# Kernel optimization log

Measured on AMD Instinct MI355X. Metric: run time of the kernel, lower is better.

## Reference

```python
import jax, jax.numpy as jnp
import numpy as np

B, C, N, H = 2, 512, 2048, 8
DK = C // H  # 64


def entmax15(z):
    """Exact 1.5-entmax over last axis (Peters & Martins 2019, sort-based)."""
    z = z / 2.0
    z = z - jnp.max(z, axis=-1, keepdims=True)
    zs = -jnp.sort(-z, axis=-1)  # descending sort
    n = zs.shape[-1]
    rho = jnp.arange(1, n + 1, dtype=z.dtype)
    mean = jnp.cumsum(zs, axis=-1) / rho
    mean_sq = jnp.cumsum(zs * zs, axis=-1) / rho
    ss = rho * (mean_sq - mean * mean)
    delta = (1.0 - ss) / rho
    tau = mean - jnp.sqrt(jnp.clip(delta, 1e-12))
    support = jnp.sum((tau <= zs).astype(jnp.int32), axis=-1)
    tau_star = jnp.take_along_axis(tau, (support - 1)[..., None], axis=-1)
    return jnp.square(jnp.clip(z - tau_star, 0.0))


def layernorm(x, a, b, eps=1e-6):
    # matches the custom LayerNorm: unbiased std (torch default), eps added to std
    mean = jnp.mean(x, axis=-1, keepdims=True)
    std = jnp.sqrt(jnp.var(x, axis=-1, ddof=1, keepdims=True))
    return a * (x - mean) / (std + eps) + b


def setup_inputs() -> dict:
    key = jax.random.key(0)
    ks = jax.random.split(key, 7)
    s = 1.0 / np.sqrt(C)  # torch Linear init range
    u = lambda k, shp: jax.random.uniform(k, shp, jnp.float32, -s, s)
    return {
        "x": jax.random.normal(ks[0], (B, C, N), jnp.float32),
        "Wq": u(ks[1], (C, C)), "bq": u(ks[2], (C,)),
        "Wk": u(ks[3], (C, C)), "bk": u(ks[4], (C,)),
        "Wv": u(ks[5], (C, C)), "bv": u(ks[6], (C,)),
        "a2": jnp.ones((C,), jnp.float32),
        "b2": jnp.ones((C,), jnp.float32),
    }


def reference(x, Wq, bq, Wk, bk, Wv, bv, a2, b2):
    xt = jnp.transpose(x, (0, 2, 1))  # (B, N, C)
    x_res = xt

    def heads(W, bias):
        y = xt @ W.T + bias  # torch Linear: x @ W.T + b
        return jnp.transpose(y.reshape(B, N, H, DK), (0, 2, 1, 3))  # (B,H,N,DK)

    q, k, v = heads(Wq, bq), heads(Wk, bk), heads(Wv, bv)
    energy = jnp.einsum("bhqd,bhkd->bhqk", q, k) / np.sqrt(DK)
    p = entmax15(energy)  # sparse attention weights
    o = jnp.einsum("bhqk,bhkd->bhqd", p, v)
    o = jnp.transpose(o, (0, 2, 1, 3)).reshape(B, N, C)
    # dropouts are identity in eval mode
    return x_res + layernorm(o, a2, b2)
```

## Files before the change

### kernel.cpp

```cpp
#include <hip/hip_runtime.h>

typedef _Float16 f16;
typedef _Float16 f16x2 __attribute__((ext_vector_type(2)));
typedef _Float16 f16x4 __attribute__((ext_vector_type(4)));
typedef _Float16 f16x8 __attribute__((ext_vector_type(8)));
typedef float    f32x4 __attribute__((ext_vector_type(4)));

#define B_  2
#define C_  512
#define N_  2048
#define H_  8
#define DK_ 64
#define BH_ 16
#define NIT 8

static __device__ __forceinline__ f16x2 cvt_pk(float a, float b) {
  return __builtin_bit_cast(f16x2, __builtin_amdgcn_cvt_pkrtz(a, b));
}

#if defined(__has_builtin)
#if __has_builtin(__builtin_amdgcn_fdot2)
#define FDOT2(a,b,c) __builtin_amdgcn_fdot2((a),(b),(c),false)
#endif
#endif
#ifndef FDOT2
static __device__ __forceinline__ float FDOT2(f16x2 a, f16x2 b, float c) {
  return c + (float)a[0]*(float)b[0] + (float)a[1]*(float)b[1];
}
#endif

#define MFMA16(a,b,acc) __builtin_amdgcn_mfma_f32_16x16x32_f16((a),(b),(acc),0,0,0)

__global__ __launch_bounds__(256) void prep_x(const float* __restrict__ x,
                                              f16* __restrict__ xT)
{
  const int nt = blockIdx.x, mt = blockIdx.y, b = blockIdx.z;
  const int n0 = nt * 64, m0 = mt * 64;
  __shared__ float tile[64][65];
  const int t = threadIdx.x;
  {
    const int ml = t >> 2, nc = (t & 3) * 16;
    const float* src = x + ((size_t)(b * C_ + m0 + ml)) * N_ + n0 + nc;
    *(float4*)&tile[ml][nc]      = *(const float4*)(src);
    *(float4*)&tile[ml][nc + 4]  = *(const float4*)(src + 4);
    *(float4*)&tile[ml][nc + 8]  = *(const float4*)(src + 8);
    *(float4*)&tile[ml][nc + 12] = *(const float4*)(src + 12);
  }
  __syncthreads();
  {
    const int nl = t >> 2, mc = (t & 3) * 16;
    f16x8 o0, o1;
    #pragma unroll
    for (int i = 0; i < 8; ++i) {
      o0[i] = (f16)tile[mc + i][nl];
      o1[i] = (f16)tile[mc + 8 + i][nl];
    }
    f16* dst = xT + ((size_t)(b * N_ + n0 + nl)) * C_ + m0 + mc;
    *(f16x8*)(dst)     = o0;
    *(f16x8*)(dst + 8) = o1;
  }
}

__global__ __launch_bounds__(256) void qkv_lds(
    const f16* __restrict__ xT,
    const float* __restrict__ Wq, const float* __restrict__ Wk,
    const float* __restrict__ Wv,
    const float* __restrict__ bq, const float* __restrict__ bk,
    const float* __restrict__ bv,
    f16* __restrict__ q16, f16* __restrict__ k16, f16* __restrict__ vT16)
{
  const int nt = blockIdx.x, ctb = blockIdx.y, z = blockIdx.z;
  const int b = z / 3, mat = z % 3;
  const float* W    = (mat == 0) ? Wq : (mat == 1) ? Wk : Wv;
  const float* bias = (mat == 0) ? bq : (mat == 1) ? bk : bv;
  const int n0 = nt * 128, c0 = ctb * 64;

  __shared__ f16 As[128 * 64];
  __shared__ f16 Bs[64 * 64];

  const int t = threadIdx.x, w = t >> 6, lane = t & 63;
  const int c = lane & 15, g = lane >> 4;

  const int rB0 = t >> 3, dS = t & 7;
  const int rB1 = rB0 + 32;
  const f16* aSrc[4];
  #pragma unroll
  for (int u = 0; u < 4; ++u) {
    const int r = rB0 + 32 * u;
    aSrc[u] = xT + (size_t)(b * N_ + n0 + r) * C_ + 8 * (dS ^ (r & 7));
  }
  const float* wSrc0 = W + (size_t)(c0 + rB0) * C_ + 8 * (dS ^ (rB0 & 7));
  const float* wSrc1 = W + (size_t)(c0 + rB1) * C_ + 8 * (dS ^ (rB1 & 7));

  f32x4 acc[2][4] = {};
  #pragma unroll 1
  for (int k0 = 0; k0 < C_; k0 += 64) {
    #pragma unroll
    for (int u = 0; u < 4; ++u)
      *(f16x8*)&As[(rB0 + 32 * u) * 64 + 8 * dS] = *(const f16x8*)(aSrc[u] + k0);
    {
      float4 u0 = *(const float4*)(wSrc0 + k0);
      float4 u1 = *(const float4*)(wSrc0 + k0 + 4);
      union { f16x8 v8; f16x2 v2[4]; } u;
      u.v2[0] = cvt_pk(u0.x, u0.y); u.v2[1] = cvt_pk(u0.z, u0.w);
      u.v2[2] = cvt_pk(u1.x, u1.y); u.v2[3] = cvt_pk(u1.z, u1.w);
      *(f16x8*)&Bs[rB0 * 64 + 8 * dS] = u.v8;
    }
    {
      float4 u0 = *(const float4*)(wSrc1 + k0);
      float4 u1 = *(const float4*)(wSrc1 + k0 + 4);
      union { f16x8 v8; f16x2 v2[4]; } u;
      u.v2[0] = cvt_pk(u0.x, u0.y); u.v2[1] = cvt_pk(u0.z, u0.w);
      u.v2[2] = cvt_pk(u1.x, u1.y); u.v2[3] = cvt_pk(u1.z, u1.w);
      *(f16x8*)&Bs[rB1 * 64 + 8 * dS] = u.v8;
    }
    __syncthreads();
    const int ar0 = 32 * w + c, ar1 = ar0 + 16;
    f16x8 a00 = *(const f16x8*)&As[ar0 * 64 + 8 * (g ^ (ar0 & 7))];
    f16x8 a01 = *(const f16x8*)&As[ar0 * 64 + 8 * ((4 + g) ^ (ar0 & 7))];
    f16x8 a10 = *(const f16x8*)&As[ar1 * 64 + 8 * (g ^ (ar1 & 7))];
    f16x8 a11 = *(const f16x8*)&As[ar1 * 64 + 8 * ((4 + g) ^ (ar1 & 7))];
    #pragma unroll
    for (int ct = 0; ct < 4; ++ct) {
      const int br = ct * 16 + c;
      f16x8 b0 = *(const f16x8*)&Bs[br * 64 + 8 * (g ^ (br & 7))];
      f16x8 b1 = *(const f16x8*)&Bs[br * 64 + 8 * ((4 + g) ^ (br & 7))];
      acc[0][ct] = MFMA16(a00, b0, acc[0][ct]);
      acc[0][ct] = MFMA16(a01, b1, acc[0][ct]);
      acc[1][ct] = MFMA16(a10, b0, acc[1][ct]);
      acc[1][ct] = MFMA16(a11, b1, acc[1][ct]);
    }
    __syncthreads();
  }

  #pragma unroll
  for (int rf = 0; rf < 2; ++rf) {
    const int nOut = n0 + 32 * w + 16 * rf + 4 * g;
    #pragma unroll
    for (int ct = 0; ct < 4; ++ct) {
      const int ccol = c0 + ct * 16 + c;
      const float bb = bias[ccol];
      if (mat == 2) {
        const int base = n0 + 32 * w;
        f16* vrow = vT16 + ((size_t)(b * C_ + ccol)) * N_ + base + 8 * g + rf;
        #pragma unroll
        for (int e = 0; e < 4; ++e)
          vrow[2 * e] = (f16)(acc[rf][ct][e] + bb);
      } else {
        const int h = ccol >> 6, d = ccol & 63;
        f16* out = (mat == 0) ? q16 : k16;
        const float sc = (mat == 0) ? 0.0625f : 1.0f;
        #pragma unroll
        for (int e = 0; e < 4; ++e)
          out[((size_t)((b * H_ + h) * N_ + nOut + e)) * DK_ + d] =
              (f16)((acc[rf][ct][e] + bb) * sc);
      }
    }
  }
}

__global__ __launch_bounds__(256, 4) void attn(
    const f16* __restrict__ q16, const f16* __restrict__ k16,
    const f16* __restrict__ vT16, float* __restrict__ o)
{
  const int bh = blockIdx.y;
  const int n0 = blockIdx.x * 16;
  const int t = threadIdx.x;
  const int w = t >> 6, lane = t & 63;
  const int c = lane & 15, g = lane >> 4;

  __shared__ f16 p_lds[16 * 520];
  __shared__ float red[2][4][16][2];

  const f16* Q  = q16  + (size_t)bh * N_ * DK_;
  const f16* K  = k16  + (size_t)bh * N_ * DK_;
  const f16* VT = vT16 + (size_t)bh * DK_ * N_;

  f16x8 qa0 = *(const f16x8*)(Q + (size_t)(n0 + c) * DK_ + 8 * g);
  f16x8 qa1 = *(const f16x8*)(Q + (size_t)(n0 + c) * DK_ + 32 + 8 * g);

  const int jbase = w * 512;

  f16x2 z2[64];
  #pragma unroll
  for (int tt = 0; tt < 16; ++tt) {
    const f16* kp0 = K + (size_t)(jbase + 32 * tt + c) * DK_ + 8 * g;
    f16x8 kb00 = *(const f16x8*)(kp0);
    f16x8 kb01 = *(const f16x8*)(kp0 + 32);
    f16x8 kb10 = *(const f16x8*)(kp0 + 16 * DK_);
    f16x8 kb11 = *(const f16x8*)(kp0 + 16 * DK_ + 32);
    f32x4 a0 = {}, a1 = {};
    a0 = MFMA16(qa0, kb00, a0);
    a0 = MFMA16(qa1, kb01, a0);
    a1 = MFMA16(qa0, kb10, a1);
    a1 = MFMA16(qa1, kb11, a1);
    #pragma unroll
    for (int e = 0; e < 4; ++e)
      z2[tt * 4 + e] = cvt_pk(a0[e], a1[e]);
  }

  f16x2 m2[4];
  #pragma unroll
  for (int e = 0; e < 4; ++e) m2[e] = z2[e];
  #pragma unroll
  for (int tt = 1; tt < 16; ++tt)
    #pragma unroll
    for (int e = 0; e < 4; ++e)
      m2[e] = __builtin_elementwise_max(m2[e], z2[tt * 4 + e]);
  float m[4];
  #pragma unroll
  for (int e = 0; e < 4; ++e) m[e] = fmaxf((float)m2[e][0], (float)m2[e][1]);
  #pragma unroll
  for (int dm = 1; dm <= 8; dm <<= 1)
    #pragma unroll
    for (int e = 0; e < 4; ++e) m[e] = fmaxf(m[e], __shfl_xor(m[e], dm, 64));
  if (c == 0) {
    #pragma unroll
    for (int e = 0; e < 4; ++e) red[0][w][4 * g + e][0] = m[e];
  }
  __syncthreads();
  #pragma unroll
  for (int e = 0; e < 4; ++e) {
    const int r = 4 * g + e;
    m[e] = fmaxf(fmaxf(red[0][0][r][0], red[0][1][r][0]),
                 fmaxf(red[0][2][r][0], red[0][3][r][0]));
  }

  float tau[4];
  #pragma unroll
  for (int e = 0; e < 4; ++e) tau[e] = m[e] - 1.f;

  const f16x2 one2  = {(_Float16)1.f, (_Float16)1.f};
  const f16x2 zero2 = {(_Float16)0.f, (_Float16)0.f};

  #pragma unroll 1
  for (int it = 0; it < NIT; ++it) {
    const int pb = (it + 1) & 1;
    f16x2 tau2[4];
    #pragma unroll
    for (int e = 0; e < 4; ++e)
      tau2[e] = cvt_pk(tau[e], tau[e]);
    float S1[4] = {0.f, 0.f, 0.f, 0.f}, S2[4] = {0.f, 0.f, 0.f, 0.f};
    #pragma unroll
    for (int tt = 0; tt < 16; ++tt)
      #pragma unroll
      for (int e = 0; e < 4; ++e) {
        f16x2 d2 = z2[tt * 4 + e] - tau2[e];
        d2 = __builtin_elementwise_max(d2, zero2);
        S1[e] = FDOT2(d2, one2, S1[e]);
        S2[e] = FDOT2(d2, d2, S2[e]);
      }
    #pragma unroll
    for (int dm = 1; dm <= 8; dm <<= 1)
      #pragma unroll
      for (int e = 0; e < 4; ++e) {
        S1[e] += __shfl_xor(S1[e], dm, 64);
        S2[e] += __shfl_xor(S2[e], dm, 64);
      }
    if (c == 0) {
      #pragma unroll
      for (int e = 0; e < 4; ++e) {
        red[pb][w][4 * g + e][0] = S1[e];
        red[pb][w][4 * g + e][1] = S2[e];
      }
    }
    __syncthreads();
    #pragma unroll
    for (int e = 0; e < 4; ++e) {
      const int r = 4 * g + e;
      float s1 = red[pb][0][r][0] + red[pb][1][r][0] + red[pb][2][r][0] + red[pb][3][r][0];
      float s2 = red[pb][0][r][1] + red[pb][1][r][1] + red[pb][2][r][1] + red[pb][3][r][1];
      tau[e] = fminf(tau[e] + (s2 - 1.f) / (2.f * s1 + 1e-20f), m[e] - 0.01f);
    }
  }

  {
    f16x2 tau2[4];
    #pragma unroll
    for (int e = 0; e < 4; ++e)
      tau2[e] = cvt_pk(tau[e], tau[e]);
    #pragma unroll
    for (int tt = 0; tt < 16; ++tt)
      #pragma unroll
      for (int e = 0; e < 4; ++e) {
        f16x2 d2 = z2[tt * 4 + e] - tau2[e];
        d2 = __builtin_elementwise_max(d2, zero2);
        z2[tt * 4 + e] = d2 * d2;
      }
  }

  f32x4 oacc = {};
  #pragma unroll 1
  for (int q = 0; q < 4; ++q) {
    if (w == q) {
      #pragma unroll
      for (int tt = 0; tt < 16; ++tt)
        #pragma unroll
        for (int e = 0; e < 4; ++e) {
          const int row = 4 * g + e;
          *(f16x2*)&p_lds[row * 520 + 32 * tt + 2 * c] = z2[tt * 4 + e];
        }
    }
    __syncthreads();
    #pragma unroll
    for (int T = 0; T < 16; ++T) {
      f16x8 pa = *(f16x8*)&p_lds[c * 520 + 32 * T + 8 * g];
      f16x8 vb = *(const f16x8*)(VT + (size_t)(16 * w + c) * N_ + 512 * q + 32 * T + 8 * g);
      oacc = MFMA16(pa, vb, oacc);
    }
    __syncthreads();
  }

  const int b = bh >> 3, h = bh & 7;
  #pragma unroll
  for (int e = 0; e < 4; ++e)
    o[((size_t)b * N_ + n0 + 4 * g + e) * C_ + h * 64 + 16 * w + c] = oacc[e];
}

__global__ __launch_bounds__(256) void ln_res(
    const float* __restrict__ o, const float* __restrict__ x,
    const float* __restrict__ a2, const float* __restrict__ b2,
    float* __restrict__ out)
{
  const int row0 = blockIdx.x * 8;
  const int b = row0 >> 11, nl = row0 & (N_ - 1);
  const int t = threadIdx.x;
  __shared__ float xres[8][516];
  {
    #pragma unroll
    for (int rep = 0; rep < 2; ++rep) {
      const int cc = t + rep * 256;
      const float* xp = x + ((size_t)(b * C_ + cc)) * N_ + nl;
      float4 u0 = *(const float4*)(xp);
      float4 u1 = *(const float4*)(xp + 4);
      xres[0][cc] = u0.x; xres[1][cc] = u0.y; xres[2][cc] = u0.z; xres[3][cc] = u0.w;
      xres[4][cc] = u1.x; xres[5][cc] = u1.y; xres[6][cc] = u1.z; xres[7][cc] = u1.w;
    }
  }
  __syncthreads();
  const int w = t >> 6, lane = t & 63;
  #pragma unroll
  for (int rr = 0; rr < 2; ++rr) {
    const int r = w * 2 + rr;
    const size_t row = (size_t)row0 + r;
    float v[8];
    #pragma unroll
    for (int i = 0; i < 8; ++i) v[i] = o[row * C_ + lane + 64 * i];
    float s = 0.f, ss = 0.f;
    #pragma unroll
    for (int i = 0; i < 8; ++i) { s += v[i]; ss = fmaf(v[i], v[i], ss); }
    #pragma unroll
    for (int dm = 1; dm <= 32; dm <<= 1) {
      s  += __shfl_xor(s, dm, 64);
      ss += __shfl_xor(ss, dm, 64);
    }
    const float mean = s * (1.f / C_);
    float var = (ss - (float)C_ * mean * mean) * (1.f / (C_ - 1));
    var = fmaxf(var, 0.f);
    const float rd = 1.f / (sqrtf(var) + 1e-6f);
    #pragma unroll
    for (int i = 0; i < 8; ++i) {
      const int cc = lane + 64 * i;
      out[row * C_ + cc] = a2[cc] * (v[i] - mean) * rd + b2[cc] + xres[r][cc];
    }
  }
}

extern "C" void kernel_launch(void* const* d_in, const int* in_sizes, int n_in,
                              void* d_out, int out_size, void* d_ws, size_t ws_size,
                              hipStream_t stream)
{
  const float* x  = (const float*)d_in[0];
  const float* Wq = (const float*)d_in[1];
  const float* bq = (const float*)d_in[2];
  const float* Wk = (const float*)d_in[3];
  const float* bk = (const float*)d_in[4];
  const float* Wv = (const float*)d_in[5];
  const float* bv = (const float*)d_in[6];
  const float* a2 = (const float*)d_in[7];
  const float* b2 = (const float*)d_in[8];

  const size_t HEADSZ = (size_t)BH_ * N_ * DK_;
  f16* q16  = (f16*)d_ws;
  f16* k16  = q16 + HEADSZ;
  f16* vT16 = k16 + HEADSZ;

  f16* xT16 = (f16*)d_out;
  float* o  = (float*)d_out;

  prep_x <<<dim3(32, 8, 2),  256, 0, stream>>>(x, xT16);
  qkv_lds<<<dim3(16, 8, 6),  256, 0, stream>>>(xT16, Wq, Wk, Wv, bq, bk, bv,
                                               q16, k16, vT16);
  attn   <<<dim3(N_ / 16, BH_), 256, 0, stream>>>(q16, k16, vT16, o);
  ln_res <<<dim3(512),       256, 0, stream>>>(o, x, a2, b2, (float*)d_out);
}
```

Baseline: 231.8 us.

## Store Q/K/V in MFMA-fragment-tiled layout and interleave heads in attention grid

```diff
diff --git a/kernel.cpp b/kernel.cpp
--- a/kernel.cpp
+++ b/kernel.cpp
@@ -30,6 +30,7 @@
 #endif
 
 #define MFMA16(a,b,acc) __builtin_amdgcn_mfma_f32_16x16x32_f16((a),(b),(acc),0,0,0)
+
 
 __global__ __launch_bounds__(256) void prep_x(const float* __restrict__ x,
                                               f16* __restrict__ xT)
@@ -135,25 +136,30 @@
 
   #pragma unroll
   for (int rf = 0; rf < 2; ++rf) {
-    const int nOut = n0 + 32 * w + 16 * rf + 4 * g;
     #pragma unroll
     for (int ct = 0; ct < 4; ++ct) {
       const int ccol = c0 + ct * 16 + c;
       const float bb = bias[ccol];
+      const int h2 = ccol >> 6;
+      const int bh = b * H_ + h2;
       if (mat == 2) {
-        const int base = n0 + 32 * w;
-        f16* vrow = vT16 + ((size_t)(b * C_ + ccol)) * N_ + base + 8 * g + rf;
+        const int dih = ccol & 63, dt = dih >> 4, cp = dih & 15;
+        const int jc = (n0 + 32 * w) >> 5;
+        f16* vp = vT16 + (((size_t)(bh * 4 + dt)) * 64 + jc) * 512
+                       + 128 * g + 8 * cp + rf;
         #pragma unroll
         for (int e = 0; e < 4; ++e)
-          vrow[2 * e] = (f16)(acc[rf][ct][e] + bb);
+          vp[2 * e] = (f16)(acc[rf][ct][e] + bb);
       } else {
-        const int h = ccol >> 6, d = ccol & 63;
+        const int d = ccol & 63, kk = d >> 5, gp = (d >> 3) & 3, ii = d & 7;
+        const int jt = (n0 + 32 * w + 16 * rf) >> 4;
         f16* out = (mat == 0) ? q16 : k16;
         const float sc = (mat == 0) ? 0.0625f : 1.0f;
+        f16* op = out + (((size_t)(bh * 128 + jt)) * 2 + kk) * 512
+                      + 128 * gp + 32 * g + ii;
         #pragma unroll
         for (int e = 0; e < 4; ++e)
-          out[((size_t)((b * H_ + h) * N_ + nOut + e)) * DK_ + d] =
-              (f16)((acc[rf][ct][e] + bb) * sc);
+          op[8 * e] = (f16)((acc[rf][ct][e] + bb) * sc);
       }
     }
   }
@@ -163,8 +169,9 @@
     const f16* __restrict__ q16, const f16* __restrict__ k16,
     const f16* __restrict__ vT16, float* __restrict__ o)
 {
-  const int bh = blockIdx.y;
-  const int n0 = blockIdx.x * 16;
+  const int id = blockIdx.x;
+  const int bh = id & 15;
+  const int n0 = (id >> 4) * 16;
   const int t = threadIdx.x;
   const int w = t >> 6, lane = t & 63;
   const int c = lane & 15, g = lane >> 4;
@@ -172,23 +179,22 @@
   __shared__ f16 p_lds[16 * 520];
   __shared__ float red[2][4][16][2];
 
-  const f16* Q  = q16  + (size_t)bh * N_ * DK_;
-  const f16* K  = k16  + (size_t)bh * N_ * DK_;
-  const f16* VT = vT16 + (size_t)bh * DK_ * N_;
-
-  f16x8 qa0 = *(const f16x8*)(Q + (size_t)(n0 + c) * DK_ + 8 * g);
-  f16x8 qa1 = *(const f16x8*)(Q + (size_t)(n0 + c) * DK_ + 32 + 8 * g);
-
-  const int jbase = w * 512;
+  const f16* Qb = q16  + (size_t)bh * (128 * 2 * 512);
+  const f16* Kb = k16  + (size_t)bh * (128 * 2 * 512);
+  const f16* Vb = vT16 + (size_t)bh * (4 * 64 * 512);
+
+  const f16* qp = Qb + (size_t)(n0 >> 4) * 1024 + 8 * lane;
+  f16x8 qa0 = *(const f16x8*)(qp);
+  f16x8 qa1 = *(const f16x8*)(qp + 512);
 
   f16x2 z2[64];
   #pragma unroll
   for (int tt = 0; tt < 16; ++tt) {
-    const f16* kp0 = K + (size_t)(jbase + 32 * tt + c) * DK_ + 8 * g;
-    f16x8 kb00 = *(const f16x8*)(kp0);
-    f16x8 kb01 = *(const f16x8*)(kp0 + 32);
-    f16x8 kb10 = *(const f16x8*)(kp0 + 16 * DK_);
-    f16x8 kb11 = *(const f16x8*)(kp0 + 16 * DK_ + 32);
+    const f16* kp = Kb + (size_t)(32 * w + 2 * tt) * 1024 + 8 * lane;
+    f16x8 kb00 = *(const f16x8*)(kp);
+    f16x8 kb01 = *(const f16x8*)(kp + 512);
+    f16x8 kb10 = *(const f16x8*)(kp + 1024);
+    f16x8 kb11 = *(const f16x8*)(kp + 1536);
     f32x4 a0 = {}, a1 = {};
     a0 = MFMA16(qa0, kb00, a0);
     a0 = MFMA16(qa1, kb01, a0);
@@ -305,7 +311,7 @@
     #pragma unroll
     for (int T = 0; T < 16; ++T) {
       f16x8 pa = *(f16x8*)&p_lds[c * 520 + 32 * T + 8 * g];
-      f16x8 vb = *(const f16x8*)(VT + (size_t)(16 * w + c) * N_ + 512 * q + 32 * T + 8 * g);
+      f16x8 vb = *(const f16x8*)(Vb + ((size_t)w * 64 + 16 * q + T) * 512 + 8 * lane);
       oacc = MFMA16(pa, vb, oacc);
     }
     __syncthreads();
@@ -391,6 +397,6 @@
   prep_x <<<dim3(32, 8, 2),  256, 0, stream>>>(x, xT16);
   qkv_lds<<<dim3(16, 8, 6),  256, 0, stream>>>(xT16, Wq, Wk, Wv, bq, bk, bv,
                                                q16, k16, vT16);
-  attn   <<<dim3(N_ / 16, BH_), 256, 0, stream>>>(q16, k16, vT16, o);
+  attn   <<<dim3(2048),      256, 0, stream>>>(q16, k16, vT16, o);
   ln_res <<<dim3(512),       256, 0, stream>>>(o, x, a2, b2, (float*)d_out);
 }
```

Result: faster. 186.2 us (-19.7%).
